# Optimization experiments

Hardware: AMD Instinct MI355X
Metric: run time of the kernel (lower is better)

Reference implementation:

```python
import jax, jax.numpy as jnp
import numpy as np

NUM_EXPERTS = 64
TOP_K = 8
HIDDEN = 2048
FFN = 768
BATCH, SEQ = 1, 2048
CAP_FACTOR = 2  # capacity = CAP_FACTOR * avg tokens/expert; >> any realistic max load


def setup_inputs() -> dict:
    key = jax.random.key(0)
    k1, k2, k3, k4, k5 = jax.random.split(key, 5)
    hidden_states = jax.random.normal(k1, (BATCH, SEQ, HIDDEN), dtype=jnp.float32)
    gate_w = jax.random.normal(k2, (NUM_EXPERTS, HIDDEN), dtype=jnp.float32) * 0.02
    w_gate = jax.random.normal(k3, (NUM_EXPERTS, FFN, HIDDEN), dtype=jnp.float32) * 0.02
    w_up = jax.random.normal(k4, (NUM_EXPERTS, FFN, HIDDEN), dtype=jnp.float32) * 0.02
    w_down = jax.random.normal(k5, (NUM_EXPERTS, HIDDEN, FFN), dtype=jnp.float32) * 0.02
    return {"hidden_states": hidden_states, "gate_w": gate_w,
            "w_gate": w_gate, "w_up": w_up, "w_down": w_down}


def _moe_forward(hidden_states, gate_w, w_gate, w_up, w_down):
    B, S, D = hidden_states.shape
    E = gate_w.shape[0]
    x = hidden_states.reshape(-1, D)                      # [N, D]
    N = x.shape[0]
    P = N * TOP_K
    C = CAP_FACTOR * P // E                               # per-expert capacity

    logits = x @ gate_w.T                                 # [N, E]
    probs = jax.nn.softmax(logits, axis=-1)
    scores, idx = jax.lax.top_k(probs, TOP_K)             # [N, K], [N, K]

    # Group (token, k) pairs by expert id for a grouped-GEMM style dispatch.
    flat_e = idx.reshape(-1)                              # [P]
    order = jnp.argsort(flat_e)                           # stable group-by expert
    e_sorted = flat_e[order]                              # [P]
    tok_sorted = order // TOP_K                           # [P] source token per pair
    s_sorted = scores.reshape(-1)[order]                  # [P]

    counts = jnp.bincount(e_sorted, length=E)             # tokens per expert
    starts = jnp.cumsum(counts) - counts                  # exclusive cumsum
    pos = jnp.arange(P) - starts[e_sorted]                # slot within expert bucket
    valid = pos < C                                       # capacity guard (never hit at these sizes)
    safe_pos = jnp.minimum(pos, C - 1)

    # Dispatch: [E, C, D] buffer of routed tokens.
    xbuf = jnp.zeros((E, C, D), dtype=x.dtype).at[e_sorted, pos].set(
        x[tok_sorted], mode="drop")

    # Batched SwiGLU FFN per expert: down( silu(gate(x)) * up(x) )
    g = jnp.einsum("ecd,efd->ecf", xbuf, w_gate)
    u = jnp.einsum("ecd,efd->ecf", xbuf, w_up)
    y = jnp.einsum("ecf,edf->ecd", jax.nn.silu(g) * u, w_down)  # [E, C, D]

    # Combine: weighted scatter-add back to token order.
    y_pair = y[e_sorted, safe_pos] * (s_sorted * valid)[:, None]  # [P, D]
    out = jnp.zeros((N, D), dtype=x.dtype).at[tok_sorted].add(y_pair)
    return out.reshape(B, S, D)


def reference(hidden_states, gate_w, w_gate, w_up, w_down):
    return _moe_forward(hidden_states, gate_w, w_gate, w_up, w_down)
```

## Files before the change

### kernel.cpp

```cpp
#include <hip/hip_runtime.h>
#include <cstdint>
#include <cstddef>

#define N_TOK 2048
#define N_EXP 64
#define TOPK  8
#define DHID  2048
#define DFFN  768
#define CAP   512

typedef short s16x8 __attribute__((ext_vector_type(8)));
typedef float f32x4 __attribute__((ext_vector_type(4)));

__device__ __forceinline__ unsigned pk_bf2(float a, float b) {
    unsigned ua = __float_as_uint(a) + 0x8000u;
    unsigned ub = __float_as_uint(b) + 0x8000u;
    return (ua >> 16) | (ub & 0xffff0000u);
}
__device__ __forceinline__ unsigned short f2bf(float a) {
    return (unsigned short)((__float_as_uint(a) + 0x8000u) >> 16);
}

__global__ __launch_bounds__(256) void k_init(float4* __restrict__ out4, int* __restrict__ counts) {
    int idx = blockIdx.x * 256 + threadIdx.x;
    const int total = (N_TOK * DHID) / 4;
    for (int i = idx; i < total; i += gridDim.x * 256)
        out4[i] = make_float4(0.f, 0.f, 0.f, 0.f);
    if (idx < N_EXP) counts[idx] = 0;
}

__global__ __launch_bounds__(256) void k_gate(const float* __restrict__ x,
                                              const float* __restrict__ gw,
                                              int* __restrict__ counts,
                                              int* __restrict__ btok,
                                              float* __restrict__ bscore) {
    __shared__ __align__(16) float xs[4][DHID];
    int t = threadIdx.x;
    int tok0 = blockIdx.x * 4;
    for (int r = 0; r < 4; ++r) {
        const float4* src = (const float4*)(x + (size_t)(tok0 + r) * DHID);
        float4* dst = (float4*)xs[r];
        for (int i = t; i < DHID / 4; i += 256) dst[i] = src[i];
    }
    __syncthreads();
    int w = t >> 6, lane = t & 63;
    int tok = tok0 + w;
    const float4* grow = (const float4*)(gw + (size_t)lane * DHID);
    const float4* xr = (const float4*)xs[w];
    float acc = 0.f;
    #pragma unroll 4
    for (int i = 0; i < DHID / 4; ++i) {
        float4 a = xr[i], b = grow[i];
        acc += a.x * b.x + a.y * b.y + a.z * b.z + a.w * b.w;
    }
    float m = acc;
    for (int o = 32; o > 0; o >>= 1) m = fmaxf(m, __shfl_xor(m, o));
    float ex = expf(acc - m);
    float sum = ex;
    for (int o = 32; o > 0; o >>= 1) sum += __shfl_xor(sum, o);
    float p = ex / sum;
    float pv = p;
    for (int k = 0; k < TOPK; ++k) {
        float mx = pv;
        for (int o = 32; o > 0; o >>= 1) mx = fmaxf(mx, __shfl_xor(mx, o));
        unsigned long long sel = __ballot(pv == mx);
        int who = __ffsll(sel) - 1;
        if (lane == who) {
            pv = -1.f;
            int pos = atomicAdd(&counts[lane], 1);
            if (pos < CAP) {
                btok[lane * CAP + pos] = tok;
                bscore[lane * CAP + pos] = p;
            }
        }
    }
}

__global__ __launch_bounds__(256) void k_gateup(const float* __restrict__ x,
                                                const float* __restrict__ wg,
                                                const float* __restrict__ wu,
                                                const int* __restrict__ counts,
                                                const int* __restrict__ btok,
                                                const float* __restrict__ bscore,
                                                unsigned short* __restrict__ h) {
    int e = blockIdx.y;
    int f0 = blockIdx.x * 64;
    int cnt = counts[e]; cnt = cnt > CAP ? CAP : cnt;
    if (cnt == 0) return;

    __shared__ unsigned short Xs[128][72];
    __shared__ unsigned short Gs[64][72];
    __shared__ unsigned short Us[64][72];
    __shared__ float Ss[128];
    __shared__ int   Ts[128];

    int t = threadIdx.x;
    int w = t >> 6, lane = t & 63;
    int wm = w & 1, wf = w >> 1;
    int row = lane & 15, quad = lane >> 4;
    int sr = t >> 1, sq = t & 1;
    int sr4 = t >> 2, sq4 = t & 3;

    const size_t wbase = ((size_t)e * DFFN + f0) * DHID;

    for (int m0 = 0; m0 < cnt; m0 += 128) {
        __syncthreads();
        if (t < 128) {
            int slot = m0 + t;
            if (slot < cnt) { Ts[t] = btok[e * CAP + slot]; Ss[t] = bscore[e * CAP + slot]; }
            else            { Ts[t] = -1;                   Ss[t] = 0.f; }
        }
        __syncthreads();

        f32x4 accg[4][2], accu[4][2];
        #pragma unroll
        for (int mi = 0; mi < 4; ++mi)
            #pragma unroll
            for (int fi = 0; fi < 2; ++fi) {
                accg[mi][fi] = f32x4{0.f, 0.f, 0.f, 0.f};
                accu[mi][fi] = f32x4{0.f, 0.f, 0.f, 0.f};
            }

        for (int k0 = 0; k0 < DHID; k0 += 64) {
            {
                int tokr = Ts[sr];
                if (tokr >= 0) {
                    const float4* src = (const float4*)(x + (size_t)tokr * DHID + k0 + sq * 32);
                    #pragma unroll
                    for (int i = 0; i < 4; ++i) {
                        float4 v0 = src[2 * i], v1 = src[2 * i + 1];
                        uint4 o;
                        o.x = pk_bf2(v0.x, v0.y); o.y = pk_bf2(v0.z, v0.w);
                        o.z = pk_bf2(v1.x, v1.y); o.w = pk_bf2(v1.z, v1.w);
                        *(uint4*)&Xs[sr][sq * 32 + i * 8] = o;
                    }
                } else {
                    uint4 z = make_uint4(0u, 0u, 0u, 0u);
                    #pragma unroll
                    for (int i = 0; i < 4; ++i) *(uint4*)&Xs[sr][sq * 32 + i * 8] = z;
                }
            }
            {
                const float4* gs = (const float4*)(wg + wbase + (size_t)sr4 * DHID + k0) + sq4 * 4;
                const float4* us = (const float4*)(wu + wbase + (size_t)sr4 * DHID + k0) + sq4 * 4;
                #pragma unroll
                for (int i = 0; i < 2; ++i) {
                    float4 v0 = gs[2 * i], v1 = gs[2 * i + 1];
                    uint4 o;
                    o.x = pk_bf2(v0.x, v0.y); o.y = pk_bf2(v0.z, v0.w);
                    o.z = pk_bf2(v1.x, v1.y); o.w = pk_bf2(v1.z, v1.w);
                    *(uint4*)&Gs[sr4][sq4 * 16 + i * 8] = o;
                }
                #pragma unroll
                for (int i = 0; i < 2; ++i) {
                    float4 v0 = us[2 * i], v1 = us[2 * i + 1];
                    uint4 o;
                    o.x = pk_bf2(v0.x, v0.y); o.y = pk_bf2(v0.z, v0.w);
                    o.z = pk_bf2(v1.x, v1.y); o.w = pk_bf2(v1.z, v1.w);
                    *(uint4*)&Us[sr4][sq4 * 16 + i * 8] = o;
                }
            }
            __syncthreads();
            #pragma unroll
            for (int kf = 0; kf < 2; ++kf) {
                s16x8 a[4];
                #pragma unroll
                for (int mi = 0; mi < 4; ++mi)
                    a[mi] = *(const s16x8*)&Xs[wm * 64 + mi * 16 + row][kf * 32 + quad * 8];
                #pragma unroll
                for (int fi = 0; fi < 2; ++fi) {
                    s16x8 bg = *(const s16x8*)&Gs[wf * 32 + fi * 16 + row][kf * 32 + quad * 8];
                    s16x8 bu = *(const s16x8*)&Us[wf * 32 + fi * 16 + row][kf * 32 + quad * 8];
                    #pragma unroll
                    for (int mi = 0; mi < 4; ++mi) {
                        accg[mi][fi] = __builtin_amdgcn_mfma_f32_16x16x32_bf16(a[mi], bg, accg[mi][fi], 0, 0, 0);
                        accu[mi][fi] = __builtin_amdgcn_mfma_f32_16x16x32_bf16(a[mi], bu, accu[mi][fi], 0, 0, 0);
                    }
                }
            }
            __syncthreads();
        }
        #pragma unroll
        for (int mi = 0; mi < 4; ++mi)
            #pragma unroll
            for (int fi = 0; fi < 2; ++fi)
                #pragma unroll
                for (int r = 0; r < 4; ++r) {
                    int sl = wm * 64 + mi * 16 + quad * 4 + r;
                    float g = accg[mi][fi][r], u = accu[mi][fi][r];
                    float hv = g * (1.f / (1.f + __expf(-g))) * u * Ss[sl];
                    size_t slot = (size_t)(m0 + sl);
                    h[((size_t)e * CAP + slot) * DFFN + f0 + wf * 32 + fi * 16 + row] = f2bf(hv);
                }
    }
}

__global__ __launch_bounds__(256) void k_down(const unsigned short* __restrict__ h,
                                              const float* __restrict__ wd,
                                              const int* __restrict__ counts,
                                              const int* __restrict__ btok,
                                              float* __restrict__ out) {
    int e = blockIdx.y;
    int d0 = blockIdx.x * 64;
    int cnt = counts[e]; cnt = cnt > CAP ? CAP : cnt;
    if (cnt == 0) return;

    __shared__ unsigned short Hs[128][72];
    __shared__ unsigned short Ws[64][72];
    __shared__ int Ts[128];

    int t = threadIdx.x;
    int w = t >> 6, lane = t & 63;
    int wm = w & 1, wdh = w >> 1;
    int row = lane & 15, quad = lane >> 4;
    int sr = t >> 1, sq = t & 1;
    int sr4 = t >> 2, sq4 = t & 3;

    const size_t wbase = ((size_t)e * DHID + d0) * DFFN;

    for (int m0 = 0; m0 < cnt; m0 += 128) {
        __syncthreads();
        if (t < 128) {
            int slot = m0 + t;
            Ts[t] = (slot < cnt) ? btok[e * CAP + slot] : -1;
        }
        __syncthreads();

        f32x4 acc[4][2];
        #pragma unroll
        for (int mi = 0; mi < 4; ++mi)
            #pragma unroll
            for (int di = 0; di < 2; ++di)
                acc[mi][di] = f32x4{0.f, 0.f, 0.f, 0.f};

        for (int k0 = 0; k0 < DFFN; k0 += 64) {
            {
                const uint4* hsrc = (const uint4*)(h + ((size_t)e * CAP + (m0 + sr)) * DFFN + k0 + sq * 32);
                #pragma unroll
                for (int i = 0; i < 4; ++i)
                    *(uint4*)&Hs[sr][sq * 32 + i * 8] = hsrc[i];
            }
            {
                const float4* dsrc = (const float4*)(wd + wbase + (size_t)sr4 * DFFN + k0) + sq4 * 4;
                #pragma unroll
                for (int i = 0; i < 2; ++i) {
                    float4 v0 = dsrc[2 * i], v1 = dsrc[2 * i + 1];
                    uint4 o;
                    o.x = pk_bf2(v0.x, v0.y); o.y = pk_bf2(v0.z, v0.w);
                    o.z = pk_bf2(v1.x, v1.y); o.w = pk_bf2(v1.z, v1.w);
                    *(uint4*)&Ws[sr4][sq4 * 16 + i * 8] = o;
                }
            }
            __syncthreads();
            #pragma unroll
            for (int kf = 0; kf < 2; ++kf) {
                s16x8 a[4];
                #pragma unroll
                for (int mi = 0; mi < 4; ++mi)
                    a[mi] = *(const s16x8*)&Hs[wm * 64 + mi * 16 + row][kf * 32 + quad * 8];
                #pragma unroll
                for (int di = 0; di < 2; ++di) {
                    s16x8 b = *(const s16x8*)&Ws[wdh * 32 + di * 16 + row][kf * 32 + quad * 8];
                    #pragma unroll
                    for (int mi = 0; mi < 4; ++mi)
                        acc[mi][di] = __builtin_amdgcn_mfma_f32_16x16x32_bf16(a[mi], b, acc[mi][di], 0, 0, 0);
                }
            }
            __syncthreads();
        }
        #pragma unroll
        for (int mi = 0; mi < 4; ++mi)
            #pragma unroll
            for (int di = 0; di < 2; ++di)
                #pragma unroll
                for (int r = 0; r < 4; ++r) {
                    int sl = wm * 64 + mi * 16 + quad * 4 + r;
                    int tok = Ts[sl];
                    if (tok >= 0)
                        atomicAdd(out + (size_t)tok * DHID + d0 + wdh * 32 + di * 16 + row,
                                  acc[mi][di][r]);
                }
    }
}

extern "C" void kernel_launch(void* const* d_in, const int* in_sizes, int n_in,
                              void* d_out, int out_size, void* d_ws, size_t ws_size,
                              hipStream_t stream) {
    const float* x  = (const float*)d_in[0];
    const float* gw = (const float*)d_in[1];
    const float* wg = (const float*)d_in[2];
    const float* wu = (const float*)d_in[3];
    const float* wd = (const float*)d_in[4];
    float* out = (float*)d_out;

    char* ws = (char*)d_ws;
    int*   counts = (int*)ws;
    int*   btok   = (int*)(ws + 4096);
    float* bscore = (float*)(ws + 4096 + 131072);
    unsigned short* h = (unsigned short*)(ws + (1 << 20));

    hipLaunchKernelGGL(k_init,   dim3(2048),   dim3(256), 0, stream, (float4*)out, counts);
    hipLaunchKernelGGL(k_gate,   dim3(N_TOK/4), dim3(256), 0, stream, x, gw, counts, btok, bscore);
    hipLaunchKernelGGL(k_gateup, dim3(12, 64), dim3(256), 0, stream, x, wg, wu, counts, btok, bscore, h);
    hipLaunchKernelGGL(k_down,   dim3(32, 64), dim3(256), 0, stream, h, wd, counts, btok, out);
}
```

Before: 1.843 ms.

## Register-prefetch next K tile and replace atomic combine with gather kernel

Both expert GEMM kernels now load the next K-slice of activations and weights into registers while MFMAs run on the current shared-memory tile. This is a software double-buffer meant to hide global load latency, and both kernels also get a two-blocks-per-CU launch bound. When the workspace is large enough, the down projection writes per-slot bf16 results to a buffer and a new combine kernel gathers each token's eight expert outputs, replacing the float atomics and the output zeroing pass. This costs extra registers, a large bf16 intermediate buffer and one more launch, and rounds y to bf16 before summing.

```diff
diff --git a/kernel.cpp b/kernel.cpp
--- a/kernel.cpp
+++ b/kernel.cpp
@@ -11,6 +11,7 @@
 
 typedef short s16x8 __attribute__((ext_vector_type(8)));
 typedef float f32x4 __attribute__((ext_vector_type(4)));
+typedef unsigned short u16x8 __attribute__((ext_vector_type(8)));
 
 __device__ __forceinline__ unsigned pk_bf2(float a, float b) {
     unsigned ua = __float_as_uint(a) + 0x8000u;
@@ -19,6 +20,13 @@
 }
 __device__ __forceinline__ unsigned short f2bf(float a) {
     return (unsigned short)((__float_as_uint(a) + 0x8000u) >> 16);
+}
+__device__ __forceinline__ float bf2f(unsigned short v) {
+    return __uint_as_float(((unsigned)v) << 16);
+}
+
+__global__ __launch_bounds__(64) void k_zero(int* __restrict__ counts) {
+    counts[threadIdx.x] = 0;
 }
 
 __global__ __launch_bounds__(256) void k_init(float4* __restrict__ out4, int* __restrict__ counts) {
@@ -33,7 +41,8 @@
                                               const float* __restrict__ gw,
                                               int* __restrict__ counts,
                                               int* __restrict__ btok,
-                                              float* __restrict__ bscore) {
+                                              float* __restrict__ bscore,
+                                              int* __restrict__ pair_slot) {
     __shared__ __align__(16) float xs[4][DHID];
     int t = threadIdx.x;
     int tok0 = blockIdx.x * 4;
@@ -68,21 +77,24 @@
         if (lane == who) {
             pv = -1.f;
             int pos = atomicAdd(&counts[lane], 1);
+            int psv = -1;
             if (pos < CAP) {
                 btok[lane * CAP + pos] = tok;
                 bscore[lane * CAP + pos] = p;
-            }
-        }
-    }
-}
-
-__global__ __launch_bounds__(256) void k_gateup(const float* __restrict__ x,
-                                                const float* __restrict__ wg,
-                                                const float* __restrict__ wu,
-                                                const int* __restrict__ counts,
-                                                const int* __restrict__ btok,
-                                                const float* __restrict__ bscore,
-                                                unsigned short* __restrict__ h) {
+                psv = lane * CAP + pos;
+            }
+            pair_slot[tok * TOPK + k] = psv;
+        }
+    }
+}
+
+__global__ __launch_bounds__(256, 2) void k_gateup(const float* __restrict__ x,
+                                                   const float* __restrict__ wg,
+                                                   const float* __restrict__ wu,
+                                                   const int* __restrict__ counts,
+                                                   const int* __restrict__ btok,
+                                                   const float* __restrict__ bscore,
+                                                   unsigned short* __restrict__ h) {
     int e = blockIdx.y;
     int f0 = blockIdx.x * 64;
     int cnt = counts[e]; cnt = cnt > CAP ? CAP : cnt;
@@ -102,6 +114,10 @@
     int sr4 = t >> 2, sq4 = t & 3;
 
     const size_t wbase = ((size_t)e * DFFN + f0) * DHID;
+    const float* gbase = wg + wbase + (size_t)sr4 * DHID;
+    const float* ubase = wu + wbase + (size_t)sr4 * DHID;
+
+    float4 pX[8], pG[4], pU[4];
 
     for (int m0 = 0; m0 < cnt; m0 += 128) {
         __syncthreads();
@@ -111,6 +127,21 @@
             else            { Ts[t] = -1;                   Ss[t] = 0.f; }
         }
         __syncthreads();
+        int tokr = Ts[sr];
+        const float4* xbase = (const float4*)(x + (size_t)(tokr < 0 ? 0 : tokr) * DHID + sq * 32);
+
+        {
+            if (tokr >= 0) {
+                #pragma unroll
+                for (int i = 0; i < 8; ++i) pX[i] = xbase[i];
+            }
+            const float4* gsrc = (const float4*)(gbase) + sq4 * 4;
+            const float4* usrc = (const float4*)(ubase) + sq4 * 4;
+            #pragma unroll
+            for (int i = 0; i < 4; ++i) pG[i] = gsrc[i];
+            #pragma unroll
+            for (int i = 0; i < 4; ++i) pU[i] = usrc[i];
+        }
 
         f32x4 accg[4][2], accu[4][2];
         #pragma unroll
@@ -122,45 +153,51 @@
             }
 
         for (int k0 = 0; k0 < DHID; k0 += 64) {
-            {
-                int tokr = Ts[sr];
-                if (tokr >= 0) {
-                    const float4* src = (const float4*)(x + (size_t)tokr * DHID + k0 + sq * 32);
-                    #pragma unroll
-                    for (int i = 0; i < 4; ++i) {
-                        float4 v0 = src[2 * i], v1 = src[2 * i + 1];
-                        uint4 o;
-                        o.x = pk_bf2(v0.x, v0.y); o.y = pk_bf2(v0.z, v0.w);
-                        o.z = pk_bf2(v1.x, v1.y); o.w = pk_bf2(v1.z, v1.w);
-                        *(uint4*)&Xs[sr][sq * 32 + i * 8] = o;
-                    }
-                } else {
-                    uint4 z = make_uint4(0u, 0u, 0u, 0u);
-                    #pragma unroll
-                    for (int i = 0; i < 4; ++i) *(uint4*)&Xs[sr][sq * 32 + i * 8] = z;
-                }
-            }
-            {
-                const float4* gs = (const float4*)(wg + wbase + (size_t)sr4 * DHID + k0) + sq4 * 4;
-                const float4* us = (const float4*)(wu + wbase + (size_t)sr4 * DHID + k0) + sq4 * 4;
-                #pragma unroll
-                for (int i = 0; i < 2; ++i) {
-                    float4 v0 = gs[2 * i], v1 = gs[2 * i + 1];
+            if (tokr >= 0) {
+                #pragma unroll
+                for (int i = 0; i < 4; ++i) {
+                    float4 v0 = pX[2 * i], v1 = pX[2 * i + 1];
                     uint4 o;
                     o.x = pk_bf2(v0.x, v0.y); o.y = pk_bf2(v0.z, v0.w);
                     o.z = pk_bf2(v1.x, v1.y); o.w = pk_bf2(v1.z, v1.w);
-                    *(uint4*)&Gs[sr4][sq4 * 16 + i * 8] = o;
+                    *(uint4*)&Xs[sr][sq * 32 + i * 8] = o;
                 }
-                #pragma unroll
-                for (int i = 0; i < 2; ++i) {
-                    float4 v0 = us[2 * i], v1 = us[2 * i + 1];
-                    uint4 o;
-                    o.x = pk_bf2(v0.x, v0.y); o.y = pk_bf2(v0.z, v0.w);
-                    o.z = pk_bf2(v1.x, v1.y); o.w = pk_bf2(v1.z, v1.w);
-                    *(uint4*)&Us[sr4][sq4 * 16 + i * 8] = o;
+            } else {
+                uint4 z = make_uint4(0u, 0u, 0u, 0u);
+                #pragma unroll
+                for (int i = 0; i < 4; ++i) *(uint4*)&Xs[sr][sq * 32 + i * 8] = z;
+            }
+            #pragma unroll
+            for (int i = 0; i < 2; ++i) {
+                float4 v0 = pG[2 * i], v1 = pG[2 * i + 1];
+                uint4 o;
+                o.x = pk_bf2(v0.x, v0.y); o.y = pk_bf2(v0.z, v0.w);
+                o.z = pk_bf2(v1.x, v1.y); o.w = pk_bf2(v1.z, v1.w);
+                *(uint4*)&Gs[sr4][sq4 * 16 + i * 8] = o;
+            }
+            #pragma unroll
+            for (int i = 0; i < 2; ++i) {
+                float4 v0 = pU[2 * i], v1 = pU[2 * i + 1];
+                uint4 o;
+                o.x = pk_bf2(v0.x, v0.y); o.y = pk_bf2(v0.z, v0.w);
+                o.z = pk_bf2(v1.x, v1.y); o.w = pk_bf2(v1.z, v1.w);
+                *(uint4*)&Us[sr4][sq4 * 16 + i * 8] = o;
+            }
+            __syncthreads();
+            int kn = k0 + 64;
+            if (kn < DHID) {
+                if (tokr >= 0) {
+                    const float4* src = xbase + kn / 4;
+                    #pragma unroll
+                    for (int i = 0; i < 8; ++i) pX[i] = src[i];
                 }
-            }
-            __syncthreads();
+                const float4* gsrc = (const float4*)(gbase + kn) + sq4 * 4;
+                const float4* usrc = (const float4*)(ubase + kn) + sq4 * 4;
+                #pragma unroll
+                for (int i = 0; i < 4; ++i) pG[i] = gsrc[i];
+                #pragma unroll
+                for (int i = 0; i < 4; ++i) pU[i] = usrc[i];
+            }
             #pragma unroll
             for (int kf = 0; kf < 2; ++kf) {
                 s16x8 a[4];
@@ -195,11 +232,13 @@
     }
 }
 
-__global__ __launch_bounds__(256) void k_down(const unsigned short* __restrict__ h,
-                                              const float* __restrict__ wd,
-                                              const int* __restrict__ counts,
-                                              const int* __restrict__ btok,
-                                              float* __restrict__ out) {
+template <bool USE_Y>
+__global__ __launch_bounds__(256, 2) void k_down(const unsigned short* __restrict__ h,
+                                                 const float* __restrict__ wd,
+                                                 const int* __restrict__ counts,
+                                                 const int* __restrict__ btok,
+                                                 unsigned short* __restrict__ y,
+                                                 float* __restrict__ out) {
     int e = blockIdx.y;
     int d0 = blockIdx.x * 64;
     int cnt = counts[e]; cnt = cnt > CAP ? CAP : cnt;
@@ -217,14 +256,28 @@
     int sr4 = t >> 2, sq4 = t & 3;
 
     const size_t wbase = ((size_t)e * DHID + d0) * DFFN;
+    const float* dbase = wd + wbase + (size_t)sr4 * DFFN;
+
+    uint4  pH[4];
+    float4 pW[4];
 
     for (int m0 = 0; m0 < cnt; m0 += 128) {
         __syncthreads();
-        if (t < 128) {
+        if (USE_Y) {
+        } else if (t < 128) {
             int slot = m0 + t;
             Ts[t] = (slot < cnt) ? btok[e * CAP + slot] : -1;
         }
         __syncthreads();
+
+        const uint4* hbase = (const uint4*)(h + ((size_t)e * CAP + (m0 + sr)) * DFFN + sq * 32);
+        {
+            #pragma unroll
+            for (int i = 0; i < 4; ++i) pH[i] = hbase[i];
+            const float4* dsrc = (const float4*)(dbase) + sq4 * 4;
+            #pragma unroll
+            for (int i = 0; i < 4; ++i) pW[i] = dsrc[i];
+        }
 
         f32x4 acc[4][2];
         #pragma unroll
@@ -234,24 +287,27 @@
                 acc[mi][di] = f32x4{0.f, 0.f, 0.f, 0.f};
 
         for (int k0 = 0; k0 < DFFN; k0 += 64) {
-            {
-                const uint4* hsrc = (const uint4*)(h + ((size_t)e * CAP + (m0 + sr)) * DFFN + k0 + sq * 32);
-                #pragma unroll
-                for (int i = 0; i < 4; ++i)
-                    *(uint4*)&Hs[sr][sq * 32 + i * 8] = hsrc[i];
-            }
-            {
-                const float4* dsrc = (const float4*)(wd + wbase + (size_t)sr4 * DFFN + k0) + sq4 * 4;
-                #pragma unroll
-                for (int i = 0; i < 2; ++i) {
-                    float4 v0 = dsrc[2 * i], v1 = dsrc[2 * i + 1];
-                    uint4 o;
-                    o.x = pk_bf2(v0.x, v0.y); o.y = pk_bf2(v0.z, v0.w);
-                    o.z = pk_bf2(v1.x, v1.y); o.w = pk_bf2(v1.z, v1.w);
-                    *(uint4*)&Ws[sr4][sq4 * 16 + i * 8] = o;
-                }
+            #pragma unroll
+            for (int i = 0; i < 4; ++i)
+                *(uint4*)&Hs[sr][sq * 32 + i * 8] = pH[i];
+            #pragma unroll
+            for (int i = 0; i < 2; ++i) {
+                float4 v0 = pW[2 * i], v1 = pW[2 * i + 1];
+                uint4 o;
+                o.x = pk_bf2(v0.x, v0.y); o.y = pk_bf2(v0.z, v0.w);
+                o.z = pk_bf2(v1.x, v1.y); o.w = pk_bf2(v1.z, v1.w);
+                *(uint4*)&Ws[sr4][sq4 * 16 + i * 8] = o;
             }
             __syncthreads();
+            int kn = k0 + 64;
+            if (kn < DFFN) {
+                const uint4* hsrc = hbase + kn / 8;
+                #pragma unroll
+                for (int i = 0; i < 4; ++i) pH[i] = hsrc[i];
+                const float4* dsrc = (const float4*)(dbase + kn) + sq4 * 4;
+                #pragma unroll
+                for (int i = 0; i < 4; ++i) pW[i] = dsrc[i];
+            }
             #pragma unroll
             for (int kf = 0; kf < 2; ++kf) {
                 s16x8 a[4];
@@ -268,18 +324,58 @@
             }
             __syncthreads();
         }
+        if (USE_Y) {
+            #pragma unroll
+            for (int mi = 0; mi < 4; ++mi)
+                #pragma unroll
+                for (int di = 0; di < 2; ++di)
+                    #pragma unroll
+                    for (int r = 0; r < 4; ++r) {
+                        int sl = wm * 64 + mi * 16 + quad * 4 + r;
+                        size_t slot = (size_t)e * CAP + (m0 + sl);
+                        y[slot * DHID + d0 + wdh * 32 + di * 16 + row] = f2bf(acc[mi][di][r]);
+                    }
+        } else {
+            #pragma unroll
+            for (int mi = 0; mi < 4; ++mi)
+                #pragma unroll
+                for (int di = 0; di < 2; ++di)
+                    #pragma unroll
+                    for (int r = 0; r < 4; ++r) {
+                        int sl = wm * 64 + mi * 16 + quad * 4 + r;
+                        int tok = Ts[sl];
+                        if (tok >= 0)
+                            atomicAdd(out + (size_t)tok * DHID + d0 + wdh * 32 + di * 16 + row,
+                                      acc[mi][di][r]);
+                    }
+        }
+    }
+}
+
+__global__ __launch_bounds__(256) void k_combine(const unsigned short* __restrict__ y,
+                                                 const int* __restrict__ pair_slot,
+                                                 float* __restrict__ out) {
+    int w = threadIdx.x >> 6, lane = threadIdx.x & 63;
+    int tok = blockIdx.x * 4 + w;
+    int slots[TOPK];
+    #pragma unroll
+    for (int k = 0; k < TOPK; ++k) slots[k] = pair_slot[tok * TOPK + k];
+    for (int c0 = 0; c0 < DHID; c0 += 512) {
+        int c = c0 + lane * 8;
+        float acc[8] = {0.f, 0.f, 0.f, 0.f, 0.f, 0.f, 0.f, 0.f};
         #pragma unroll
-        for (int mi = 0; mi < 4; ++mi)
-            #pragma unroll
-            for (int di = 0; di < 2; ++di)
-                #pragma unroll
-                for (int r = 0; r < 4; ++r) {
-                    int sl = wm * 64 + mi * 16 + quad * 4 + r;
-                    int tok = Ts[sl];
-                    if (tok >= 0)
-                        atomicAdd(out + (size_t)tok * DHID + d0 + wdh * 32 + di * 16 + row,
-                                  acc[mi][di][r]);
-                }
+        for (int k = 0; k < TOPK; ++k) {
+            int s = slots[k];
+            if (s >= 0) {
+                u16x8 v = *(const u16x8*)(y + (size_t)s * DHID + c);
+                #pragma unroll
+                for (int j = 0; j < 8; ++j) acc[j] += bf2f(v[j]);
+            }
+        }
+        float4 o0 = make_float4(acc[0], acc[1], acc[2], acc[3]);
+        float4 o1 = make_float4(acc[4], acc[5], acc[6], acc[7]);
+        *(float4*)(out + (size_t)tok * DHID + c)     = o0;
+        *(float4*)(out + (size_t)tok * DHID + c + 4) = o1;
     }
 }
 
@@ -294,13 +390,27 @@
     float* out = (float*)d_out;
 
     char* ws = (char*)d_ws;
-    int*   counts = (int*)ws;
-    int*   btok   = (int*)(ws + 4096);
-    float* bscore = (float*)(ws + 4096 + 131072);
+    int*   counts    = (int*)ws;
+    int*   btok      = (int*)(ws + 4096);
+    float* bscore    = (float*)(ws + 4096 + 131072);
+    int*   pair_slot = (int*)(ws + 4096 + 262144);
     unsigned short* h = (unsigned short*)(ws + (1 << 20));
-
-    hipLaunchKernelGGL(k_init,   dim3(2048),   dim3(256), 0, stream, (float4*)out, counts);
-    hipLaunchKernelGGL(k_gate,   dim3(N_TOK/4), dim3(256), 0, stream, x, gw, counts, btok, bscore);
-    hipLaunchKernelGGL(k_gateup, dim3(12, 64), dim3(256), 0, stream, x, wg, wu, counts, btok, bscore, h);
-    hipLaunchKernelGGL(k_down,   dim3(32, 64), dim3(256), 0, stream, h, wd, counts, btok, out);
-}
+    unsigned short* y = (unsigned short*)(ws + (1 << 20) + (size_t)N_EXP * CAP * DFFN * 2);
+
+    const size_t need_big = (1 << 20) + (size_t)N_EXP * CAP * DFFN * 2
+                                      + (size_t)N_EXP * CAP * DHID * 2;
+    const bool bigws = ws_size >= need_big;
+
+    if (bigws) {
+        k_zero<<<1, 64, 0, stream>>>(counts);
+        k_gate<<<N_TOK / 4, 256, 0, stream>>>(x, gw, counts, btok, bscore, pair_slot);
+        k_gateup<<<dim3(12, 64), 256, 0, stream>>>(x, wg, wu, counts, btok, bscore, h);
+        k_down<true><<<dim3(32, 64), 256, 0, stream>>>(h, wd, counts, btok, y, out);
+        k_combine<<<N_TOK / 4, 256, 0, stream>>>(y, pair_slot, out);
+    } else {
+        k_init<<<2048, 256, 0, stream>>>((float4*)out, counts);
+        k_gate<<<N_TOK / 4, 256, 0, stream>>>(x, gw, counts, btok, bscore, pair_slot);
+        k_gateup<<<dim3(12, 64), 256, 0, stream>>>(x, wg, wu, counts, btok, bscore, h);
+        k_down<false><<<dim3(32, 64), 256, 0, stream>>>(h, wd, counts, btok, nullptr, out);
+    }
+}
```

Result: slower. 2.121 ms (+15.1%).
